# Kernel tuning notes

Measured on AMD Instinct MI355X. Metric: run time of the kernel, lower is better.

The kernel has to match this reference:

```python
import jax, jax.numpy as jnp
import numpy as np

N, E, IN, H, D = 50000, 800000, 128, 2, 64  # heads=2, head_dim=64, hidden*2 = 128


def setup_inputs() -> dict:
    key = jax.random.key(0)
    ks = jax.random.split(key, 8)
    s = 1.0 / np.sqrt(IN)
    return {
        "x": jax.random.normal(ks[0], (N, IN), dtype=jnp.float32),
        "edge_index": jax.random.randint(ks[1], (2, E), 0, N, dtype=jnp.int64),
        "Wq": jax.random.normal(ks[2], (IN, H * D), dtype=jnp.float32) * s,
        "bq": jnp.zeros((H * D,), jnp.float32),
        "Wk": jax.random.normal(ks[3], (IN, H * D), dtype=jnp.float32) * s,
        "bk": jnp.zeros((H * D,), jnp.float32),
        "Wv": jax.random.normal(ks[4], (IN, H * D), dtype=jnp.float32) * s,
        "bv": jnp.zeros((H * D,), jnp.float32),
        "Wskip": jax.random.normal(ks[5], (IN, H * D), dtype=jnp.float32) * s,
        "bskip": jnp.zeros((H * D,), jnp.float32),
        "Wdec": jax.random.normal(ks[6], (H * D, IN), dtype=jnp.float32) * (1.0 / np.sqrt(H * D)),
        "bdec": jnp.zeros((IN,), jnp.float32),
    }


def reference(x, edge_index, Wq, bq, Wk, bk, Wv, bv, Wskip, bskip, Wdec, bdec):
    n = x.shape[0]
    src, dst = edge_index[0], edge_index[1]  # message flows src -> dst (PyG convention)
    q = (x @ Wq + bq).reshape(n, H, D)
    k = (x @ Wk + bk).reshape(n, H, D)
    v = (x @ Wv + bv).reshape(n, H, D)
    # per-edge multi-head scores [E, H]
    score = jnp.einsum('ehd,ehd->eh', q[dst], k[src]) / jnp.sqrt(jnp.asarray(D, x.dtype))
    # segment softmax over in-edges of each destination node
    m = jax.ops.segment_max(score, dst, num_segments=n)
    m = jnp.where(jnp.isfinite(m), m, jnp.zeros_like(m))  # nodes with no in-edges
    e = jnp.exp(score - m[dst])
    denom = jax.ops.segment_sum(e, dst, num_segments=n) + 1e-16
    alpha = e / denom[dst]                      # [E, H]
    msg = v[src] * alpha[..., None]             # [E, H, D]
    agg = jax.ops.segment_sum(msg, dst, num_segments=n)  # [N, H, D]
    z = agg.reshape(n, H * D) + (x @ Wskip + bskip)       # concat heads + root skip
    x_hat = z @ Wdec + bdec
    return (x_hat, z)
```

## Files before the change

### kernel.cpp

```cpp
#include <hip/hip_runtime.h>
#include <hip/hip_bf16.h>
#include <math.h>

typedef unsigned short u16;
typedef unsigned char u8;
typedef unsigned int u32;
typedef __attribute__((ext_vector_type(8))) short bf16x8;
typedef __attribute__((ext_vector_type(4))) float f32x4;

__device__ __forceinline__ float b2f(u16 u) {
  union { unsigned int i; float f; } x; x.i = ((unsigned int)u) << 16; return x.f;
}
__device__ __forceinline__ u16 f2b(float f) {
  union { float f; unsigned int i; } x; x.f = f;
  unsigned int r = x.i + 0x7FFFu + ((x.i >> 16) & 1u);
  return (u16)(r >> 16);
}
__device__ __forceinline__ float4 cvt4(ushort4 u) {
  return make_float4(b2f(u.x), b2f(u.y), b2f(u.z), b2f(u.w));
}
__device__ __forceinline__ float4 i8x4_to_f4(u32 w) {
  return make_float4((float)((int)(w << 24) >> 24), (float)((int)(w << 16) >> 24),
                     (float)((int)(w << 8) >> 24), (float)((int)w >> 24));
}

#if __has_builtin(__builtin_amdgcn_sdot4)
__device__ __forceinline__ int dot4i8(u32 a, u32 b) {
  return __builtin_amdgcn_sdot4((int)a, (int)b, 0, false);
}
#else
__device__ __forceinline__ int dot4i8(u32 a, u32 b) {
  int s = ((int)(a << 24) >> 24) * ((int)(b << 24) >> 24);
  s += ((int)(a << 16) >> 24) * ((int)(b << 16) >> 24);
  s += ((int)(a << 8) >> 24) * ((int)(b << 8) >> 24);
  s += ((int)a >> 24) * ((int)b >> 24);
  return s;
}
#endif

__device__ __forceinline__ bool ei_is_i64(const int* __restrict__ ei) {
  return (ei[1] | ei[3] | ei[5] | ei[7] | ei[9] | ei[11] | ei[13] | ei[15]) == 0;
}

__global__ __launch_bounds__(256) void wprep_kernel(
    const float* __restrict__ Wq, const float* __restrict__ Wk,
    const float* __restrict__ Wv, const float* __restrict__ Wsk,
    const float* __restrict__ Wd,
    const float* __restrict__ bq, const float* __restrict__ bk,
    const float* __restrict__ bv, const float* __restrict__ bsk,
    const float* __restrict__ bd,
    short* __restrict__ Wt, float* __restrict__ bias,
    int* __restrict__ cnt, int n) {
  int g = blockIdx.x * 256 + threadIdx.x;
  if (g < 5 * 16384) {
    int mat = g >> 14, rem = g & 16383;
    int frag = rem >> 9;
    int l = (rem >> 3) & 63;
    int j = rem & 7;
    int nt = frag >> 2, s = frag & 3;
    int nrow = nt * 16 + (l & 15);
    int kcol = s * 32 + (l >> 4) * 8 + j;
    const float* W = (mat == 0) ? Wq : (mat == 1) ? Wk : (mat == 2) ? Wv
                     : (mat == 3) ? Wsk : Wd;
    float scl = (mat == 0) ? 0.125f : 1.f;
    Wt[g] = (short)f2b(W[kcol * 128 + nrow] * scl);
  }
  if (g < 5 * 128) {
    int mat = g >> 7, nn = g & 127;
    const float* B = (mat == 0) ? bq : (mat == 1) ? bk : (mat == 2) ? bv
                     : (mat == 3) ? bsk : bd;
    bias[g] = B[nn] * ((mat == 0) ? 0.125f : 1.f);
  }
  if (g < n) cnt[g] = 0;
}

__global__ __launch_bounds__(256) void count_kernel(const int* __restrict__ ei,
                                                    int* __restrict__ cnt,
                                                    u8* __restrict__ rank, int E) {
  int e = blockIdx.x * 256 + threadIdx.x;
  bool f = ei_is_i64(ei);
  if (e < E) {
    int idx = f ? (e << 1) : e;
    int dbase = f ? (E << 1) : E;
    int d = ei[dbase + idx];
    rank[e] = (u8)atomicAdd(&cnt[d], 1);
  }
}

__global__ __launch_bounds__(1024) void scanA_kernel(const int* __restrict__ cnt,
                                                     int* __restrict__ offs,
                                                     int* __restrict__ parts, int n) {
  __shared__ int wsum[16];
  int i = blockIdx.x * 1024 + threadIdx.x;
  int lane = threadIdx.x & 63, wid = threadIdx.x >> 6;
  int v = (i < n) ? cnt[i] : 0;
  int s = v;
#pragma unroll
  for (int off = 1; off < 64; off <<= 1) {
    int t = __shfl_up(s, off, 64);
    if (lane >= off) s += t;
  }
  if (lane == 63) wsum[wid] = s;
  __syncthreads();
  if (threadIdx.x == 0) {
    int acc = 0;
#pragma unroll
    for (int w = 0; w < 16; ++w) { int t = wsum[w]; wsum[w] = acc; acc += t; }
    parts[blockIdx.x] = acc;
  }
  __syncthreads();
  if (i < n) offs[i] = wsum[wid] + (s - v);
}

__global__ __launch_bounds__(1024) void scanC_kernel(int* __restrict__ offs,
                                                     const int* __restrict__ parts,
                                                     int n, int nb) {
  __shared__ int sh[2];
  if (threadIdx.x < 64) {
    int lane = threadIdx.x;
    int v = (lane < nb) ? parts[lane] : 0;
    int s = v;
#pragma unroll
    for (int off = 1; off < 64; off <<= 1) {
      int t = __shfl_up(s, off, 64);
      if (lane >= off) s += t;
    }
    int base = __shfl(s - v, blockIdx.x, 64);
    int tot  = __shfl(s, nb - 1, 64);
    if (lane == 0) { sh[0] = base; sh[1] = tot; }
  }
  __syncthreads();
  int i = blockIdx.x * 1024 + threadIdx.x;
  if (i < n) offs[i] += sh[0];
  if (i == 0) offs[n] = sh[1];
}

__global__ __launch_bounds__(256) void scatter_kernel(const int* __restrict__ ei,
                                                      const int* __restrict__ offs,
                                                      const u8* __restrict__ rank,
                                                      int* __restrict__ csr, int E) {
  int e = blockIdx.x * 256 + threadIdx.x;
  bool f = ei_is_i64(ei);
  if (e < E) {
    int idx = f ? (e << 1) : e;
    int dbase = f ? (E << 1) : E;
    int s = ei[idx];
    int d = ei[dbase + idx];
    int pos = offs[d] + (int)rank[e];
    __builtin_nontemporal_store(s, &csr[pos]);
  }
}

__global__ __launch_bounds__(512) void proj_kernel(const float* __restrict__ x,
    const short* __restrict__ Wt, const float* __restrict__ bias,
    u32* __restrict__ q8, float* __restrict__ qscb,
    u32* __restrict__ kvq, float* __restrict__ scb,
    u32* __restrict__ skip32, int n) {
  __shared__ short xt[32 * 128];
  __shared__ u32 qsL[32 * 33];
  __shared__ u32 kvL[32 * 65];
  __shared__ u32 skL[32 * 65];
  __shared__ float qscL[32 * 2];
  __shared__ float scL[32 * 4];
  int m0 = blockIdx.x * 32;
  int tid = threadIdx.x;
  {
    int row = tid >> 4, c = tid & 15;
    int grow = m0 + row;
    bf16x8 val;
    if (grow < n) {
      const float* sp = x + (size_t)grow * 128 + c * 8;
      float4 f0 = *(const float4*)sp;
      float4 f1 = *(const float4*)(sp + 4);
      val[0] = (short)f2b(f0.x); val[1] = (short)f2b(f0.y);
      val[2] = (short)f2b(f0.z); val[3] = (short)f2b(f0.w);
      val[4] = (short)f2b(f1.x); val[5] = (short)f2b(f1.y);
      val[6] = (short)f2b(f1.z); val[7] = (short)f2b(f1.w);
    } else {
#pragma unroll
      for (int j = 0; j < 8; ++j) val[j] = 0;
    }
    *(bf16x8*)&xt[row * 128 + ((c ^ (row & 15)) << 3)] = val;
  }
  __syncthreads();

  int wid = tid >> 6, l = tid & 63;
  int mat = wid & 3, mhalf = wid >> 2;
  int lm = l & 15, lk = l >> 4;
  const short* Wl = Wt + (size_t)mat * 16384 + l * 8;
  int ml = mhalf * 16 + lm;
  f32x4 acc[8];
#pragma unroll
  for (int nt = 0; nt < 8; ++nt) acc[nt] = (f32x4){0.f, 0.f, 0.f, 0.f};

#pragma unroll
  for (int s = 0; s < 4; ++s) {
    int c = s * 4 + lk;
    bf16x8 bfrag = *(const bf16x8*)&xt[ml * 128 + ((c ^ (ml & 15)) << 3)];
#pragma unroll
    for (int nt = 0; nt < 8; ++nt) {
      bf16x8 afrag = *(const bf16x8*)(Wl + nt * 2048 + s * 512);
      acc[nt] = __builtin_amdgcn_mfma_f32_16x16x32_bf16(afrag, bfrag, acc[nt], 0, 0, 0);
    }
  }

  const float* bs = bias + mat * 128;
#pragma unroll
  for (int nt = 0; nt < 8; ++nt) {
    float4 b4 = *(const float4*)(bs + nt * 16 + lk * 4);
    acc[nt][0] += b4.x; acc[nt][1] += b4.y;
    acc[nt][2] += b4.z; acc[nt][3] += b4.w;
  }
  int lrow = mhalf * 16 + lm;
  if (mat < 3) {
#pragma unroll
    for (int h = 0; h < 2; ++h) {
      float am = 0.f;
#pragma unroll
      for (int nt4 = 0; nt4 < 4; ++nt4) {
        int nt = h * 4 + nt4;
#pragma unroll
        for (int j = 0; j < 4; ++j) am = fmaxf(am, fabsf(acc[nt][j]));
      }
      am = fmaxf(am, __shfl_xor(am, 16));
      am = fmaxf(am, __shfl_xor(am, 32));
      float inv = (am > 0.f) ? 127.f / am : 0.f;
#pragma unroll
      for (int nt4 = 0; nt4 < 4; ++nt4) {
        int nt = h * 4 + nt4;
        u32 pk = 0;
#pragma unroll
        for (int j = 0; j < 4; ++j) {
          float qv = fminf(fmaxf(rintf(acc[nt][j] * inv), -127.f), 127.f);
          pk |= ((u32)((int)qv & 0xff)) << (8 * j);
        }
        int slot = nt4 * 4 + lk;
        if (mat == 0) qsL[lrow * 33 + h * 16 + slot] = pk;
        else kvL[lrow * 65 + h * 32 + slot * 2 + (mat - 1)] = pk;
      }
      if (lk == 0) {
        float sc = am * (1.f / 127.f);
        if (mat == 0) qscL[lrow * 2 + h] = sc;
        else scL[lrow * 4 + h * 2 + (mat - 1)] = sc;
      }
    }
  } else {
#pragma unroll
    for (int nt = 0; nt < 8; ++nt) {
      u16 o0 = f2b(acc[nt][0]), o1 = f2b(acc[nt][1]);
      u16 o2 = f2b(acc[nt][2]), o3 = f2b(acc[nt][3]);
      int u = nt * 8 + lk * 2;
      skL[lrow * 65 + u]     = (u32)o0 | ((u32)o1 << 16);
      skL[lrow * 65 + u + 1] = (u32)o2 | ((u32)o3 << 16);
    }
  }
  __syncthreads();

  int nvalid = n - m0; if (nvalid > 32) nvalid = 32;
  for (int idx = tid; idx < nvalid * 32; idx += 512) {
    int node = idx >> 5, slot = idx & 31;
    q8[(size_t)(m0 + node) * 32 + slot] = qsL[node * 33 + slot];
  }
  for (int idx = tid; idx < nvalid * 64; idx += 512) {
    int node = idx >> 6, slot = idx & 63;
    kvq[(size_t)(m0 + node) * 64 + slot] = kvL[node * 65 + slot];
  }
  for (int idx = tid; idx < nvalid * 64; idx += 512) {
    int node = idx >> 6, slot = idx & 63;
    skip32[(size_t)(m0 + node) * 64 + slot] = skL[node * 65 + slot];
  }
  for (int idx = tid; idx < nvalid * 4; idx += 512) {
    int node = idx >> 2, s = idx & 3;
    scb[(size_t)(m0 + node) * 4 + s] = scL[node * 4 + s];
  }
  for (int idx = tid; idx < nvalid * 2; idx += 512) {
    int node = idx >> 1, h = idx & 1;
    qscb[(size_t)(m0 + node) * 2 + h] = qscL[node * 2 + h];
  }
}

__global__ __launch_bounds__(256) void dec_kernel(const float* __restrict__ zin,
    const short* __restrict__ Wt, const float* __restrict__ bias,
    float* __restrict__ out, int n) {
  __shared__ short zt[128 * 128];
  int m0 = blockIdx.x * 128;
  int tid = threadIdx.x;
#pragma unroll
  for (int p = 0; p < 8; ++p) {
    int cid = tid + p * 256;
    int row = cid >> 4, c = cid & 15;
    int grow = m0 + row;
    bf16x8 val;
    if (grow < n) {
      const float* sp = zin + (size_t)grow * 128 + c * 8;
      float4 f0 = *(const float4*)sp;
      float4 f1 = *(const float4*)(sp + 4);
      val[0] = (short)f2b(f0.x); val[1] = (short)f2b(f0.y);
      val[2] = (short)f2b(f0.z); val[3] = (short)f2b(f0.w);
      val[4] = (short)f2b(f1.x); val[5] = (short)f2b(f1.y);
      val[6] = (short)f2b(f1.z); val[7] = (short)f2b(f1.w);
    } else {
#pragma unroll
      for (int j = 0; j < 8; ++j) val[j] = 0;
    }
    *(bf16x8*)&zt[row * 128 + ((c ^ (row & 15)) << 3)] = val;
  }
  __syncthreads();

  int wid = tid >> 6, l = tid & 63;
  int lm = l & 15, lk = l >> 4;
  int mbase = wid * 32;
  const short* Wl = Wt + l * 8;
  f32x4 acc[2][8];
#pragma unroll
  for (int mt = 0; mt < 2; ++mt)
#pragma unroll
    for (int nt = 0; nt < 8; ++nt) acc[mt][nt] = (f32x4){0.f, 0.f, 0.f, 0.f};

#pragma unroll
  for (int s = 0; s < 4; ++s) {
    bf16x8 bfrag[2];
#pragma unroll
    for (int mt = 0; mt < 2; ++mt) {
      int ml = mbase + mt * 16 + lm;
      int c = s * 4 + lk;
      bfrag[mt] = *(const bf16x8*)&zt[ml * 128 + ((c ^ (ml & 15)) << 3)];
    }
#pragma unroll
    for (int nt = 0; nt < 8; ++nt) {
      bf16x8 afrag = *(const bf16x8*)(Wl + nt * 2048 + s * 512);
      acc[0][nt] = __builtin_amdgcn_mfma_f32_16x16x32_bf16(afrag, bfrag[0], acc[0][nt], 0, 0, 0);
      acc[1][nt] = __builtin_amdgcn_mfma_f32_16x16x32_bf16(afrag, bfrag[1], acc[1][nt], 0, 0, 0);
    }
  }

#pragma unroll
  for (int mt = 0; mt < 2; ++mt) {
    int m = m0 + mbase + mt * 16 + lm;
    if (m >= n) continue;
#pragma unroll
    for (int nt = 0; nt < 8; ++nt) {
      int n4 = nt * 16 + lk * 4;
      float4 b4 = *(const float4*)(bias + n4);
      f32x4 a = acc[mt][nt];
      *(float4*)(out + (size_t)m * 128 + n4) =
          make_float4(a[0] + b4.x, a[1] + b4.y, a[2] + b4.z, a[3] + b4.w);
    }
  }
}

#define PAIR_BODY(EA, EB, SACC, AACC, HM)                                    \
  {                                                                          \
    int e_ = half ? (EB) : (EA);                                             \
    u32 kvoff_ = (u32)e_ * 256u + (u32)(l32 * 8);                            \
    uint2 kv_ = *(const uint2*)(kvbytes + kvoff_);                           \
    float2 sc_ = *(const float2*)(scbytes + (u32)e_ * 16u + (u32)(h * 8));   \
    int pi_ = dot4i8(qw, kv_.x);                                             \
    pi_ += __shfl_xor(pi_, 1);                                               \
    pi_ += __shfl_xor(pi_, 2);                                               \
    pi_ += __shfl_xor(pi_, 4);                                               \
    pi_ += __shfl_xor(pi_, 8);                                               \
    float w_ = __expf((float)pi_ * (qs * sc_.x)) * (HM);                     \
    float4 vv_ = i8x4_to_f4(kv_.y);                                          \
    float wv_ = w_ * sc_.y;                                                  \
    SACC += w_;                                                              \
    AACC.x += wv_ * vv_.x; AACC.y += wv_ * vv_.y;                            \
    AACC.z += wv_ * vv_.z; AACC.w += wv_ * vv_.w;                            \
  }

__global__ __launch_bounds__(256) void attn_kernel(const u32* __restrict__ q8,
                                                   const float* __restrict__ qscb,
                                                   const u32* __restrict__ kvq,
                                                   const float* __restrict__ scb,
                                                   const u16* __restrict__ skipb,
                                                   const int* __restrict__ offs,
                                                   const int* __restrict__ csr,
                                                   float* __restrict__ z, int nn) {
  int wv = __builtin_amdgcn_readfirstlane((int)(threadIdx.x >> 6));
  int dst = blockIdx.x * 4 + wv;
  if (dst >= nn) return;
  int lane = threadIdx.x & 63;
  int half = lane >> 5;
  int l32 = lane & 31;
  int h = l32 >> 4;
  u32 qw = q8[(size_t)dst * 32 + l32];
  float qs = qscb[(size_t)dst * 2 + h];
  int i0 = __builtin_amdgcn_readfirstlane(offs[dst]);
  int i1 = __builtin_amdgcn_readfirstlane(offs[dst + 1]);
  const u8* kvbytes = (const u8*)kvq;
  const u8* scbytes = (const u8*)scb;
  float hm1 = (half == 0) ? 1.f : 0.f;

  float s0 = 0.f, s1 = 0.f, s2 = 0.f, s3 = 0.f;
  float4 A0 = {0, 0, 0, 0}, A1 = {0, 0, 0, 0}, A2 = {0, 0, 0, 0}, A3 = {0, 0, 0, 0};

  int i = i0;
  for (; i + 7 < i1; i += 8) {
    int e0 = csr[i], e1 = csr[i + 1], e2 = csr[i + 2], e3 = csr[i + 3];
    int e4 = csr[i + 4], e5 = csr[i + 5], e6 = csr[i + 6], e7 = csr[i + 7];
    PAIR_BODY(e0, e1, s0, A0, 1.f)
    PAIR_BODY(e2, e3, s1, A1, 1.f)
    PAIR_BODY(e4, e5, s2, A2, 1.f)
    PAIR_BODY(e6, e7, s3, A3, 1.f)
  }
  for (; i + 1 < i1; i += 2) {
    int e0 = csr[i], e1 = csr[i + 1];
    PAIR_BODY(e0, e1, s0, A0, 1.f)
  }
  if (i < i1) {
    int e0 = csr[i];
    PAIR_BODY(e0, e0, s0, A0, hm1)
  }

  float sum = (s0 + s1) + (s2 + s3);
  float b0 = (A0.x + A1.x) + (A2.x + A3.x);
  float b1 = (A0.y + A1.y) + (A2.y + A3.y);
  float b2 = (A0.z + A1.z) + (A2.z + A3.z);
  float b3 = (A0.w + A1.w) + (A2.w + A3.w);
  sum += __shfl_xor(sum, 32);
  b0 += __shfl_xor(b0, 32);
  b1 += __shfl_xor(b1, 32);
  b2 += __shfl_xor(b2, 32);
  b3 += __shfl_xor(b3, 32);
  if (half == 0) {
    float inv = 1.f / (sum + 1e-16f);
    int qoff = dst * 128 + h * 64 + (l32 & 15) * 4;
    float4 sk = cvt4(*(const ushort4*)(skipb + qoff));
    *(float4*)(z + qoff) = make_float4(b0 * inv + sk.x, b1 * inv + sk.y,
                                       b2 * inv + sk.z, b3 * inv + sk.w);
  }
}

extern "C" void kernel_launch(void* const* d_in, const int* in_sizes, int n_in,
                              void* d_out, int out_size, void* d_ws, size_t ws_size,
                              hipStream_t stream) {
  const float* x  = (const float*)d_in[0];
  const int*   ei = (const int*)d_in[1];
  const float* Wq = (const float*)d_in[2];
  const float* bq = (const float*)d_in[3];
  const float* Wk = (const float*)d_in[4];
  const float* bk = (const float*)d_in[5];
  const float* Wv = (const float*)d_in[6];
  const float* bv = (const float*)d_in[7];
  const float* Wsk = (const float*)d_in[8];
  const float* bsk = (const float*)d_in[9];
  const float* Wd = (const float*)d_in[10];
  const float* bd = (const float*)d_in[11];

  int N = in_sizes[0] / 128;
  int E = in_sizes[1] / 2;

  char* w = (char*)d_ws;
  auto alloc = [&](size_t bytes) {
    char* p = w;
    w += (bytes + 255) & ~(size_t)255;
    return p;
  };
  u32* q8    = (u32*)alloc((size_t)N * 32 * 4);
  float* qscb = (float*)alloc((size_t)N * 2 * 4);
  u32* kvq   = (u32*)alloc((size_t)N * 64 * 4);
  float* scb = (float*)alloc((size_t)N * 4 * 4);
  u16* skipb = (u16*)alloc((size_t)N * 128 * 2);
  int* cnt  = (int*)alloc((size_t)(N + 1) * 4);
  int* offs = (int*)alloc((size_t)(N + 1) * 4);
  u8*  rank = (u8*)alloc((size_t)E);
  int* csr  = (int*)alloc((size_t)E * 4);
  int* parts = (int*)alloc(66 * 4);
  short* Wt = (short*)alloc(5 * 16384 * 2);
  float* bias = (float*)alloc(5 * 128 * 4);

  float* xhat = (float*)d_out;
  float* z = xhat + (size_t)N * 128;

  int nb = (N + 1023) / 1024;

  wprep_kernel<<<320, 256, 0, stream>>>(Wq, Wk, Wv, Wsk, Wd, bq, bk, bv, bsk, bd,
                                        Wt, bias, cnt, N);
  count_kernel<<<(E + 255) / 256, 256, 0, stream>>>(ei, cnt, rank, E);
  scanA_kernel<<<nb, 1024, 0, stream>>>(cnt, offs, parts, N);
  scanC_kernel<<<nb, 1024, 0, stream>>>(offs, parts, N, nb);
  scatter_kernel<<<(E + 255) / 256, 256, 0, stream>>>(ei, offs, rank, csr, E);

  proj_kernel<<<(N + 31) / 32, 512, 0, stream>>>(x, Wt, bias, q8, qscb, kvq, scb,
                                                 (u32*)skipb, N);

  attn_kernel<<<(N + 3) / 4, 256, 0, stream>>>(q8, qscb, kvq, scb, skipb, offs, csr,
                                               z, N);

  dec_kernel<<<(N + 127) / 128, 256, 0, stream>>>(z, Wt + 4 * 16384, bias + 4 * 128,
                                                  xhat, N);
}
```

Baseline: 166.1 us.

## Process four edges per wave with 16-byte KV loads and biased uint8 V

The int8 K/V layout changes so that each lane reads 8 K bytes and 8 V bytes in a single 16-byte load. Each wave now handles four edges at once, one per group of 16 lanes, with 8 lanes per head, which shortens the shuffle reduction. V is stored with a +127 offset so the kernel can use the hardware unsigned-byte-to-float conversions, and the offset is removed at the end using a separately accumulated weight sum. The aim is fewer memory transactions and fewer ALU ops per edge. In exchange, partially filled quads on low-degree nodes waste lanes, and the tail is handled by masked redundant loads.

```diff
diff --git a/kernel.cpp b/kernel.cpp
--- a/kernel.cpp
+++ b/kernel.cpp
@@ -19,23 +19,31 @@
 __device__ __forceinline__ float4 cvt4(ushort4 u) {
   return make_float4(b2f(u.x), b2f(u.y), b2f(u.z), b2f(u.w));
 }
-__device__ __forceinline__ float4 i8x4_to_f4(u32 w) {
-  return make_float4((float)((int)(w << 24) >> 24), (float)((int)(w << 16) >> 24),
-                     (float)((int)(w << 8) >> 24), (float)((int)w >> 24));
-}
 
 #if __has_builtin(__builtin_amdgcn_sdot4)
-__device__ __forceinline__ int dot4i8(u32 a, u32 b) {
-  return __builtin_amdgcn_sdot4((int)a, (int)b, 0, false);
+__device__ __forceinline__ int dot4i8c(u32 a, u32 b, int c) {
+  return __builtin_amdgcn_sdot4((int)a, (int)b, c, false);
 }
 #else
-__device__ __forceinline__ int dot4i8(u32 a, u32 b) {
+__device__ __forceinline__ int dot4i8c(u32 a, u32 b, int c) {
   int s = ((int)(a << 24) >> 24) * ((int)(b << 24) >> 24);
   s += ((int)(a << 16) >> 24) * ((int)(b << 16) >> 24);
   s += ((int)(a << 8) >> 24) * ((int)(b << 8) >> 24);
   s += ((int)a >> 24) * ((int)b >> 24);
-  return s;
-}
+  return s + c;
+}
+#endif
+
+#if __has_builtin(__builtin_amdgcn_cvt_f32_ubyte0)
+#define UB0(x) __builtin_amdgcn_cvt_f32_ubyte0(x)
+#define UB1(x) __builtin_amdgcn_cvt_f32_ubyte1(x)
+#define UB2(x) __builtin_amdgcn_cvt_f32_ubyte2(x)
+#define UB3(x) __builtin_amdgcn_cvt_f32_ubyte3(x)
+#else
+#define UB0(x) ((float)((x) & 0xffu))
+#define UB1(x) ((float)(((x) >> 8) & 0xffu))
+#define UB2(x) ((float)(((x) >> 16) & 0xffu))
+#define UB3(x) ((float)(((x) >> 24) & 0xffu))
 #endif
 
 __device__ __forceinline__ bool ei_is_i64(const int* __restrict__ ei) {
@@ -213,6 +221,7 @@
   }
   int lrow = mhalf * 16 + lm;
   if (mat < 3) {
+    int vbias = (mat == 2) ? 127 : 0;
 #pragma unroll
     for (int h = 0; h < 2; ++h) {
       float am = 0.f;
@@ -232,11 +241,15 @@
 #pragma unroll
         for (int j = 0; j < 4; ++j) {
           float qv = fminf(fmaxf(rintf(acc[nt][j] * inv), -127.f), 127.f);
-          pk |= ((u32)((int)qv & 0xff)) << (8 * j);
+          pk |= ((u32)(((int)qv + vbias) & 0xff)) << (8 * j);
         }
-        int slot = nt4 * 4 + lk;
-        if (mat == 0) qsL[lrow * 33 + h * 16 + slot] = pk;
-        else kvL[lrow * 65 + h * 32 + slot * 2 + (mat - 1)] = pk;
+        if (mat == 0) {
+          qsL[lrow * 33 + h * 16 + nt4 * 4 + lk] = pk;
+        } else {
+          int d0 = nt4 * 16 + lk * 4;
+          int idx = (d0 >> 3) * 4 + ((mat == 1) ? 0 : 2) + ((d0 >> 2) & 1);
+          kvL[lrow * 65 + h * 32 + idx] = pk;
+        }
       }
       if (lk == 0) {
         float sc = am * (1.f / 127.f);
@@ -349,23 +362,24 @@
   }
 }
 
-#define PAIR_BODY(EA, EB, SACC, AACC, HM)                                    \
+#define QUAD_BODY(IBASE, SACC, S2ACC, AV)                                    \
   {                                                                          \
-    int e_ = half ? (EB) : (EA);                                             \
-    u32 kvoff_ = (u32)e_ * 256u + (u32)(l32 * 8);                            \
-    uint2 kv_ = *(const uint2*)(kvbytes + kvoff_);                           \
-    float2 sc_ = *(const float2*)(scbytes + (u32)e_ * 16u + (u32)(h * 8));   \
-    int pi_ = dot4i8(qw, kv_.x);                                             \
+    int ii_ = (IBASE) + e4;                                                  \
+    float msk_ = (ii_ < i1) ? 1.f : 0.f;                                     \
+    int e_ = csr[(ii_ < i1) ? ii_ : i0];                                     \
+    uint4 kv_ = *(const uint4*)(kvb + (u32)e_ * 256u + hb);                  \
+    float2 sc_ = *(const float2*)(scB + (u32)e_ * 16u + (u32)(h * 8));       \
+    int pi_ = dot4i8c(qw.y, kv_.y, dot4i8c(qw.x, kv_.x, 0));                 \
     pi_ += __shfl_xor(pi_, 1);                                               \
     pi_ += __shfl_xor(pi_, 2);                                               \
     pi_ += __shfl_xor(pi_, 4);                                               \
-    pi_ += __shfl_xor(pi_, 8);                                               \
-    float w_ = __expf((float)pi_ * (qs * sc_.x)) * (HM);                     \
-    float4 vv_ = i8x4_to_f4(kv_.y);                                          \
+    float w_ = __expf((float)pi_ * (qs * sc_.x)) * msk_;                     \
     float wv_ = w_ * sc_.y;                                                  \
-    SACC += w_;                                                              \
-    AACC.x += wv_ * vv_.x; AACC.y += wv_ * vv_.y;                            \
-    AACC.z += wv_ * vv_.z; AACC.w += wv_ * vv_.w;                            \
+    SACC += w_; S2ACC += wv_;                                                \
+    AV[0] += wv_ * UB0(kv_.z); AV[1] += wv_ * UB1(kv_.z);                    \
+    AV[2] += wv_ * UB2(kv_.z); AV[3] += wv_ * UB3(kv_.z);                    \
+    AV[4] += wv_ * UB0(kv_.w); AV[5] += wv_ * UB1(kv_.w);                    \
+    AV[6] += wv_ * UB2(kv_.w); AV[7] += wv_ * UB3(kv_.w);                    \
   }
 
 __global__ __launch_bounds__(256) void attn_kernel(const u32* __restrict__ q8,
@@ -380,54 +394,55 @@
   int dst = blockIdx.x * 4 + wv;
   if (dst >= nn) return;
   int lane = threadIdx.x & 63;
-  int half = lane >> 5;
-  int l32 = lane & 31;
-  int h = l32 >> 4;
-  u32 qw = q8[(size_t)dst * 32 + l32];
+  int e4 = lane >> 4;
+  int h = (lane >> 3) & 1;
+  int l8 = lane & 7;
+  uint2 qw = *(const uint2*)(q8 + (size_t)dst * 32 + h * 16 + l8 * 2);
   float qs = qscb[(size_t)dst * 2 + h];
   int i0 = __builtin_amdgcn_readfirstlane(offs[dst]);
   int i1 = __builtin_amdgcn_readfirstlane(offs[dst + 1]);
-  const u8* kvbytes = (const u8*)kvq;
-  const u8* scbytes = (const u8*)scb;
-  float hm1 = (half == 0) ? 1.f : 0.f;
-
-  float s0 = 0.f, s1 = 0.f, s2 = 0.f, s3 = 0.f;
-  float4 A0 = {0, 0, 0, 0}, A1 = {0, 0, 0, 0}, A2 = {0, 0, 0, 0}, A3 = {0, 0, 0, 0};
-
-  int i = i0;
-  for (; i + 7 < i1; i += 8) {
-    int e0 = csr[i], e1 = csr[i + 1], e2 = csr[i + 2], e3 = csr[i + 3];
-    int e4 = csr[i + 4], e5 = csr[i + 5], e6 = csr[i + 6], e7 = csr[i + 7];
-    PAIR_BODY(e0, e1, s0, A0, 1.f)
-    PAIR_BODY(e2, e3, s1, A1, 1.f)
-    PAIR_BODY(e4, e5, s2, A2, 1.f)
-    PAIR_BODY(e6, e7, s3, A3, 1.f)
-  }
-  for (; i + 1 < i1; i += 2) {
-    int e0 = csr[i], e1 = csr[i + 1];
-    PAIR_BODY(e0, e1, s0, A0, 1.f)
-  }
-  if (i < i1) {
-    int e0 = csr[i];
-    PAIR_BODY(e0, e0, s0, A0, hm1)
-  }
-
-  float sum = (s0 + s1) + (s2 + s3);
-  float b0 = (A0.x + A1.x) + (A2.x + A3.x);
-  float b1 = (A0.y + A1.y) + (A2.y + A3.y);
-  float b2 = (A0.z + A1.z) + (A2.z + A3.z);
-  float b3 = (A0.w + A1.w) + (A2.w + A3.w);
-  sum += __shfl_xor(sum, 32);
-  b0 += __shfl_xor(b0, 32);
-  b1 += __shfl_xor(b1, 32);
-  b2 += __shfl_xor(b2, 32);
-  b3 += __shfl_xor(b3, 32);
-  if (half == 0) {
-    float inv = 1.f / (sum + 1e-16f);
-    int qoff = dst * 128 + h * 64 + (l32 & 15) * 4;
-    float4 sk = cvt4(*(const ushort4*)(skipb + qoff));
-    *(float4*)(z + qoff) = make_float4(b0 * inv + sk.x, b1 * inv + sk.y,
-                                       b2 * inv + sk.z, b3 * inv + sk.w);
+  const u8* kvb = (const u8*)kvq;
+  const u8* scB = (const u8*)scb;
+  u32 hb = (u32)(h * 128 + l8 * 16);
+
+  float sA = 0.f, s2A = 0.f, sB = 0.f, s2B = 0.f;
+  float A[8], B[8];
+#pragma unroll
+  for (int j = 0; j < 8; ++j) { A[j] = 0.f; B[j] = 0.f; }
+
+  for (int i = i0; i < i1; i += 8) {
+    QUAD_BODY(i, sA, s2A, A)
+    if (i + 4 < i1) {
+      QUAD_BODY(i + 4, sB, s2B, B)
+    }
+  }
+
+  sA += sB; s2A += s2B;
+  float c127 = 127.f * s2A;
+#pragma unroll
+  for (int j = 0; j < 8; ++j) A[j] += B[j];
+#pragma unroll
+  for (int j = 0; j < 8; ++j) A[j] -= c127;
+  sA += __shfl_xor(sA, 16); sA += __shfl_xor(sA, 32);
+#pragma unroll
+  for (int j = 0; j < 8; ++j) {
+    A[j] += __shfl_xor(A[j], 16);
+    A[j] += __shfl_xor(A[j], 32);
+  }
+  if (e4 == 0) {
+    float inv = 1.f / (sA + 1e-16f);
+    int qoff = dst * 128 + h * 64 + l8 * 8;
+    uint4 sk = *(const uint4*)(skipb + qoff);
+    float4 o0 = make_float4(A[0] * inv + b2f((u16)(sk.x & 0xffff)),
+                            A[1] * inv + b2f((u16)(sk.x >> 16)),
+                            A[2] * inv + b2f((u16)(sk.y & 0xffff)),
+                            A[3] * inv + b2f((u16)(sk.y >> 16)));
+    float4 o1 = make_float4(A[4] * inv + b2f((u16)(sk.z & 0xffff)),
+                            A[5] * inv + b2f((u16)(sk.z >> 16)),
+                            A[6] * inv + b2f((u16)(sk.w & 0xffff)),
+                            A[7] * inv + b2f((u16)(sk.w >> 16)));
+    *(float4*)(z + qoff) = o0;
+    *(float4*)(z + qoff + 4) = o1;
   }
 }
 
```

Result: no change. 169.1 us (+1.8%).

## Fuse edge counting into weight prep and CSR scatter into projection kernel

Applied to the files above, without the earlier changes.

Merges the weight-prep and edge-count kernels into one launch, with the count-array zeroing moved to a memset issued beforehand. It also moves the CSR scatter loop into the start of the projection kernel as a grid-stride loop. Together these cut two kernel launches and the gaps between them. The cost is extra memory work and latency at the head of every projection block, plus the added memset call.

```diff
diff --git a/kernel.cpp b/kernel.cpp
--- a/kernel.cpp
+++ b/kernel.cpp
@@ -42,7 +42,7 @@
   return (ei[1] | ei[3] | ei[5] | ei[7] | ei[9] | ei[11] | ei[13] | ei[15]) == 0;
 }
 
-__global__ __launch_bounds__(256) void wprep_kernel(
+__global__ __launch_bounds__(256) void prep_kernel(
     const float* __restrict__ Wq, const float* __restrict__ Wk,
     const float* __restrict__ Wv, const float* __restrict__ Wsk,
     const float* __restrict__ Wd,
@@ -50,7 +50,8 @@
     const float* __restrict__ bv, const float* __restrict__ bsk,
     const float* __restrict__ bd,
     short* __restrict__ Wt, float* __restrict__ bias,
-    int* __restrict__ cnt, int n) {
+    const int* __restrict__ ei, int* __restrict__ cnt,
+    u8* __restrict__ rank, int E) {
   int g = blockIdx.x * 256 + threadIdx.x;
   if (g < 5 * 16384) {
     int mat = g >> 14, rem = g & 16383;
@@ -71,19 +72,12 @@
                      : (mat == 3) ? bsk : bd;
     bias[g] = B[nn] * ((mat == 0) ? 0.125f : 1.f);
   }
-  if (g < n) cnt[g] = 0;
-}
-
-__global__ __launch_bounds__(256) void count_kernel(const int* __restrict__ ei,
-                                                    int* __restrict__ cnt,
-                                                    u8* __restrict__ rank, int E) {
-  int e = blockIdx.x * 256 + threadIdx.x;
   bool f = ei_is_i64(ei);
-  if (e < E) {
-    int idx = f ? (e << 1) : e;
+  if (g < E) {
+    int idx = f ? (g << 1) : g;
     int dbase = f ? (E << 1) : E;
     int d = ei[dbase + idx];
-    rank[e] = (u8)atomicAdd(&cnt[d], 1);
+    rank[g] = (u8)atomicAdd(&cnt[d], 1);
   }
 }
 
@@ -135,27 +129,13 @@
   if (i == 0) offs[n] = sh[1];
 }
 
-__global__ __launch_bounds__(256) void scatter_kernel(const int* __restrict__ ei,
-                                                      const int* __restrict__ offs,
-                                                      const u8* __restrict__ rank,
-                                                      int* __restrict__ csr, int E) {
-  int e = blockIdx.x * 256 + threadIdx.x;
-  bool f = ei_is_i64(ei);
-  if (e < E) {
-    int idx = f ? (e << 1) : e;
-    int dbase = f ? (E << 1) : E;
-    int s = ei[idx];
-    int d = ei[dbase + idx];
-    int pos = offs[d] + (int)rank[e];
-    __builtin_nontemporal_store(s, &csr[pos]);
-  }
-}
-
 __global__ __launch_bounds__(512) void proj_kernel(const float* __restrict__ x,
     const short* __restrict__ Wt, const float* __restrict__ bias,
     u32* __restrict__ q8, float* __restrict__ qscb,
     u32* __restrict__ kvq, float* __restrict__ scb,
-    u32* __restrict__ skip32, int n) {
+    u32* __restrict__ skip32, int n,
+    const int* __restrict__ ei, const int* __restrict__ offs,
+    const u8* __restrict__ rank, int* __restrict__ csr, int E) {
   __shared__ short xt[32 * 128];
   __shared__ u32 qsL[32 * 33];
   __shared__ u32 kvL[32 * 65];
@@ -164,6 +144,20 @@
   __shared__ float scL[32 * 4];
   int m0 = blockIdx.x * 32;
   int tid = threadIdx.x;
+
+  {
+    bool f = ei_is_i64(ei);
+    int stride = gridDim.x * 512;
+    for (int e = blockIdx.x * 512 + tid; e < E; e += stride) {
+      int idx = f ? (e << 1) : e;
+      int dbase = f ? (E << 1) : E;
+      int s = ei[idx];
+      int d = ei[dbase + idx];
+      int pos = offs[d] + (int)rank[e];
+      __builtin_nontemporal_store(s, &csr[pos]);
+    }
+  }
+
   {
     int row = tid >> 4, c = tid & 15;
     int grow = m0 + row;
@@ -473,16 +467,18 @@
   float* z = xhat + (size_t)N * 128;
 
   int nb = (N + 1023) / 1024;
-
-  wprep_kernel<<<320, 256, 0, stream>>>(Wq, Wk, Wv, Wsk, Wd, bq, bk, bv, bsk, bd,
-                                        Wt, bias, cnt, N);
-  count_kernel<<<(E + 255) / 256, 256, 0, stream>>>(ei, cnt, rank, E);
+  int gp = (E + 255) / 256;
+  if (gp < 320) gp = 320;
+
+  hipMemsetAsync(cnt, 0, (size_t)N * 4, stream);
+  prep_kernel<<<gp, 256, 0, stream>>>(Wq, Wk, Wv, Wsk, Wd, bq, bk, bv, bsk, bd,
+                                      Wt, bias, ei, cnt, rank, E);
   scanA_kernel<<<nb, 1024, 0, stream>>>(cnt, offs, parts, N);
   scanC_kernel<<<nb, 1024, 0, stream>>>(offs, parts, N, nb);
-  scatter_kernel<<<(E + 255) / 256, 256, 0, stream>>>(ei, offs, rank, csr, E);
 
   proj_kernel<<<(N + 31) / 32, 512, 0, stream>>>(x, Wt, bias, q8, qscb, kvq, scb,
-                                                 (u32*)skipb, N);
+                                                 (u32*)skipb, N, ei, offs, rank,
+                                                 csr, E);
 
   attn_kernel<<<(N + 3) / 4, 256, 0, stream>>>(q8, qscb, kvq, scb, skipb, offs, csr,
                                                z, N);
```

After: 155.7 us (median of 2 runs). -6.2%, faster.
